# Optimization experiments

Measured on AMD Instinct MI355X. Metric: run time of the kernel, lower is better.

## Reference

```python
import jax, jax.numpy as jnp
import numpy as np
from functools import partial

FEAT = 12544  # 64 * 14 * 14, CfC input_size
UNITS = 64
BB = 128      # ncps CfC default backbone_units (backbone_layers=1)
N_ACTIONS = 8


def lecun_tanh(x):
    return 1.7159 * jnp.tanh(0.666 * x)


def setup_inputs() -> dict:
    key = jax.random.key(0)
    ks = jax.random.split(key, 20)
    s = 0.05
    inp = {
        "x": jax.random.normal(ks[0], (16, 64, 3, 62, 62), dtype=jnp.float32),
        "conv1_w": jax.random.normal(ks[1], (32, 3, 4, 4), dtype=jnp.float32) * s,
        "conv1_b": jnp.zeros((32,), dtype=jnp.float32),
        "conv2_w": jax.random.normal(ks[2], (64, 32, 4, 4), dtype=jnp.float32) * s,
        "conv2_b": jnp.zeros((64,), dtype=jnp.float32),
        "W_bb": jax.random.normal(ks[3], (FEAT + UNITS, BB), dtype=jnp.float32) * 0.01,
        "b_bb": jnp.zeros((BB,), dtype=jnp.float32),
        "W_ff1": jax.random.normal(ks[4], (BB, UNITS), dtype=jnp.float32) * s,
        "b_ff1": jnp.zeros((UNITS,), dtype=jnp.float32),
        "W_ff2": jax.random.normal(ks[5], (BB, UNITS), dtype=jnp.float32) * s,
        "b_ff2": jnp.zeros((UNITS,), dtype=jnp.float32),
        "W_ta": jax.random.normal(ks[6], (BB, UNITS), dtype=jnp.float32) * s,
        "b_ta": jnp.zeros((UNITS,), dtype=jnp.float32),
        "W_tb": jax.random.normal(ks[7], (BB, UNITS), dtype=jnp.float32) * s,
        "b_tb": jnp.zeros((UNITS,), dtype=jnp.float32),
        "W_out": jax.random.normal(ks[8], (UNITS, N_ACTIONS), dtype=jnp.float32) * s,
        "b_out": jnp.zeros((N_ACTIONS,), dtype=jnp.float32),
    }
    return inp


def _conv(x, w, b):
    y = jax.lax.conv_general_dilated(
        x, w, window_strides=(2, 2), padding="VALID",
        dimension_numbers=("NCHW", "OIHW", "NCHW"))
    return jax.nn.relu(y + b[None, :, None, None])


def reference(x, conv1_w, conv1_b, conv2_w, conv2_b, W_bb, b_bb,
              W_ff1, b_ff1, W_ff2, b_ff2, W_ta, b_ta, W_tb, b_tb,
              W_out, b_out):
    B, T, C, H, W = x.shape
    c_in = x.reshape(B * T, C, H, W)
    h = _conv(c_in, conv1_w, conv1_b)          # [BT,32,30,30]
    h = _conv(h, conv2_w, conv2_b)             # [BT,64,14,14]
    feat = h.reshape(B, T, FEAT)               # torch Flatten order == NCHW reshape

    # CfC (ncps, mode='default', backbone_layers=1, ts=1.0), return_sequences=False
    W_in, W_h = W_bb[:FEAT], W_bb[FEAT:]
    # precompute input contribution to backbone for all timesteps
    u = jnp.einsum("btf,fk->btk", feat, W_in) + b_bb   # [B,T,BB]

    def step(hid, u_t):
        z = lecun_tanh(u_t + hid @ W_h)                # backbone activation
        ff1 = jnp.tanh(z @ W_ff1 + b_ff1)
        ff2 = jnp.tanh(z @ W_ff2 + b_ff2)
        t_interp = jax.nn.sigmoid((z @ W_ta + b_ta) + (z @ W_tb + b_tb))  # ts=1.0
        hid_new = ff1 * (1.0 - t_interp) + t_interp * ff2
        return hid_new, None

    h0 = jnp.zeros((B, UNITS), dtype=x.dtype)
    h_last, _ = jax.lax.scan(step, h0, jnp.swapaxes(u, 0, 1))  # scan over time
    return h_last @ W_out + b_out
```

## Files before the change

### kernel.cpp

```cpp
#include <hip/hip_runtime.h>
#include <hip/hip_bf16.h>
#include <math.h>

#define FEATN 12544
#define NIMG 1024
#define PLANEP 482

typedef __attribute__((ext_vector_type(8))) short short8;
typedef __attribute__((ext_vector_type(4))) float f32x4;

#define OFF_W1F   0
#define OFF_W2F   6144
#define OFF_WBBF  71680
#define OFF_FEATB 62265344
#define OFF_U     87955456
#define OFF_PART  88479744
#define OFF_WHF   103163904
#define OFF_WGF   103180288
#define WS_BYTES  103245824

__device__ __forceinline__ unsigned short f2bf(float v) {
    union { float f; unsigned int u; } c; c.f = v;
    unsigned int r = c.u + 0x7FFFu + ((c.u >> 16) & 1u);
    return (unsigned short)(r >> 16);
}
__device__ __forceinline__ unsigned short f2bf_rhu(float v) {
    union { float f; unsigned int u; } c; c.f = v;
    return (unsigned short)((c.u + 0x8000u) >> 16);
}
__device__ __forceinline__ unsigned int pack2bf_rhu(float lo, float hi) {
    union { float f; unsigned int u; } a, b; a.f = lo; b.f = hi;
    return ((a.u + 0x8000u) >> 16) | ((b.u + 0x8000u) & 0xFFFF0000u);
}

__device__ __forceinline__ float lecun_tanh_fast(float x) {
    float e = __builtin_amdgcn_exp2f(1.9216698f * x);
    return 1.7159f - 3.4318f * __builtin_amdgcn_rcpf(e + 1.f);
}
__device__ __forceinline__ float tanh_fast(float x) {
    float e = __builtin_amdgcn_exp2f(2.8853901f * x);
    return 1.f - 2.f * __builtin_amdgcn_rcpf(e + 1.f);
}
__device__ __forceinline__ float sigmoid_fast(float x) {
    float e = __builtin_amdgcn_exp2f(-1.4426950f * x);
    return __builtin_amdgcn_rcpf(1.f + e);
}

__global__ __launch_bounds__(256) void prep_all(const float* __restrict__ w1, const float* __restrict__ w2,
                         const float* __restrict__ Wbb,
                         const float* __restrict__ Wff1, const float* __restrict__ Wff2,
                         const float* __restrict__ Wta,  const float* __restrict__ Wtb,
                         unsigned short* __restrict__ w1f, unsigned short* __restrict__ w2f,
                         unsigned short* __restrict__ wbbf,
                         unsigned short* __restrict__ whf, unsigned short* __restrict__ wgf) {
    int bid = blockIdx.x, tid = threadIdx.x;
    if (bid < 6272) {
        int i = bid * 256 + tid;
        int j = i & 7, lane = (i >> 3) & 63, nt = (i >> 9) & 7, kstep = i >> 12;
        int f = kstep * 32 + (lane >> 4) * 8 + j;
        int col = nt * 16 + (lane & 15);
        wbbf[i] = f2bf(Wbb[(size_t)f * 128 + col]);
    } else if (bid < 6400) {
        int i = (bid - 6272) * 256 + tid;
        int j = i & 7, lane = (i >> 3) & 63, kstep = (i >> 9) & 15, nt = i >> 13;
        int oc = nt * 16 + (lane & 15);
        int ic = 2 * kstep + (j >> 2);
        int ky = lane >> 4, kx = j & 3;
        w2f[i] = f2bf(w2[oc * 512 + ic * 16 + ky * 4 + kx]);
    } else if (bid < 6528) {
        int i = (bid - 6400) * 256 + tid;
        int j = i & 7, lane = (i >> 3) & 63, nt = (i >> 9) & 15, kstep = (i >> 13) & 3;
        int gq = (lane >> 4) & 3;
        int k = kstep * 32 + (j & 1) * 16 + gq * 4 + (j >> 1);
        int m = nt >> 2;
        int c = (nt & 3) * 16 + (lane & 15);
        float v;
        if (m == 0)      v = Wff1[k * 64 + c];
        else if (m == 1) v = Wff2[k * 64 + c];
        else if (m == 2) v = Wta[k * 64 + c] + Wtb[k * 64 + c];
        else             v = 0.f;
        wgf[i] = f2bf(v);
    } else if (bid < 6560) {
        int i = (bid - 6528) * 256 + tid;
        int j = i & 7, lane = (i >> 3) & 63, nt = (i >> 9) & 7, kstep = (i >> 12) & 1;
        int k = kstep * 32 + ((lane >> 4) & 3) * 8 + j;
        int col = nt * 16 + (lane & 15);
        whf[i] = f2bf(Wbb[(size_t)(FEATN + k) * 128 + col]);
    } else {
        int i = (bid - 6560) * 256 + tid;
        if (i >= 2048) return;
        int j = i & 7, lane = (i >> 3) & 63, nt = (i >> 9) & 1, kstep = (i >> 10) & 1;
        int oc = nt * 16 + (lane & 15);
        int ky = (lane >> 4) & 3, kx = j & 3;
        float v;
        if (kstep == 0) { int ic = j >> 2; v = w1[oc * 48 + ic * 16 + ky * 4 + kx]; }
        else            { v = (j >> 2) == 0 ? w1[oc * 48 + 32 + ky * 4 + kx] : 0.f; }
        w1f[i] = f2bf(v);
    }
}

__global__ __launch_bounds__(512) void fused_conv(const float* __restrict__ x,
                                                  const float* __restrict__ b1,
                                                  const unsigned short* __restrict__ w1f,
                                                  const float* __restrict__ b2,
                                                  const unsigned short* __restrict__ w2f,
                                                  unsigned short* __restrict__ featb) {
    __shared__ unsigned short h1s[32 * 2 * PLANEP];
    int img = blockIdx.x;
    int tid = threadIdx.x;
    int lane = tid & 63, wid = tid >> 6;
    int rowl = lane & 15, g = lane >> 4;
    const float* xg = x + (size_t)img * 11532;

    {
        short8 bfr[2][2];
        #pragma unroll
        for (int ks = 0; ks < 2; ++ks)
            #pragma unroll
            for (int nt = 0; nt < 2; ++nt)
                bfr[ks][nt] = *(const short8*)(w1f + (((ks * 2 + nt) * 64 + lane) << 3));
        float bias0 = b1[rowl], bias1 = b1[16 + rowl];

        #pragma unroll
        for (int i = 0; i < 8; ++i) {
            int mtile = wid + 8 * i;
            if (mtile >= 57) break;
            int m = mtile * 16 + rowl; if (m > 899) m = 899;
            int oy = m / 30, ox = m - oy * 30;
            int y = 2 * oy + g, x0 = 2 * ox;
            const float* xb = xg + y * 62 + x0;
            union { unsigned int u[4]; short8 s; } af0, af1;
            #pragma unroll
            for (int c = 0; c < 2; ++c) {
                float2 p0 = *(const float2*)(xb + c * 3844);
                float2 p1 = *(const float2*)(xb + c * 3844 + 2);
                af0.u[c * 2]     = pack2bf_rhu(p0.x, p0.y);
                af0.u[c * 2 + 1] = pack2bf_rhu(p1.x, p1.y);
            }
            {
                float2 q0 = *(const float2*)(xb + 7688);
                float2 q1 = *(const float2*)(xb + 7690);
                af1.u[0] = pack2bf_rhu(q0.x, q0.y);
                af1.u[1] = pack2bf_rhu(q1.x, q1.y);
                af1.u[2] = 0; af1.u[3] = 0;
            }
            f32x4 acc0 = (f32x4){0.f, 0.f, 0.f, 0.f};
            f32x4 acc1 = (f32x4){0.f, 0.f, 0.f, 0.f};
            acc0 = __builtin_amdgcn_mfma_f32_16x16x32_bf16(af0.s, bfr[0][0], acc0, 0, 0, 0);
            acc0 = __builtin_amdgcn_mfma_f32_16x16x32_bf16(af1.s, bfr[1][0], acc0, 0, 0, 0);
            acc1 = __builtin_amdgcn_mfma_f32_16x16x32_bf16(af0.s, bfr[0][1], acc1, 0, 0, 0);
            acc1 = __builtin_amdgcn_mfma_f32_16x16x32_bf16(af1.s, bfr[1][1], acc1, 0, 0, 0);
            int sp0 = mtile * 16 + g * 4;
            int oy0 = sp0 / 30, ox0 = sp0 - oy0 * 30;
            #pragma unroll
            for (int nt = 0; nt < 2; ++nt) {
                f32x4 a = nt ? acc1 : acc0;
                int oc = nt * 16 + rowl;
                float bias = nt ? bias1 : bias0;
                int pbase = oc * (2 * PLANEP);
                #pragma unroll
                for (int r = 0; r < 4; ++r) {
                    if (sp0 + r > 899) break;
                    int oxr = ox0 + r, oyr = oy0;
                    if (oxr >= 30) { oxr -= 30; ++oyr; }
                    h1s[pbase + oyr * 32 + oxr] = f2bf_rhu(fmaxf(a[r] + bias, 0.f));
                }
            }
        }
    }
    __syncthreads();

    f32x4 acc[2][4];
    #pragma unroll
    for (int i = 0; i < 2; ++i)
        #pragma unroll
        for (int nt = 0; nt < 4; ++nt) acc[i][nt] = (f32x4){0.f, 0.f, 0.f, 0.f};

    int dofs[2];
    #pragma unroll
    for (int i = 0; i < 2; ++i) {
        int mtile = wid + 8 * i;
        int m = mtile * 16 + rowl; if (m > 195) m = 195;
        int oy = m / 14, ox = m - oy * 14;
        int y = 2 * oy + g, x0 = 2 * ox;
        dofs[i] = y * 16 + (x0 >> 1);
    }
    const unsigned int* lds32 = (const unsigned int*)h1s;

    #pragma unroll 4
    for (int kstep = 0; kstep < 16; ++kstep) {
        short8 bfr[4];
        #pragma unroll
        for (int nt = 0; nt < 4; ++nt)
            bfr[nt] = *(const short8*)(w2f + (((nt * 16 + kstep) * 64 + lane) << 3));
        int icb = kstep * 2 * PLANEP;
        #pragma unroll
        for (int i = 0; i < 2; ++i) {
            int mtile = wid + 8 * i;
            if (mtile < 13) {
                int dof = icb + dofs[i];
                union { unsigned int u[4]; short8 s; } af;
                af.u[0] = lds32[dof];
                af.u[1] = lds32[dof + 1];
                af.u[2] = lds32[dof + PLANEP];
                af.u[3] = lds32[dof + PLANEP + 1];
                #pragma unroll
                for (int nt = 0; nt < 4; ++nt)
                    acc[i][nt] = __builtin_amdgcn_mfma_f32_16x16x32_bf16(af.s, bfr[nt], acc[i][nt], 0, 0, 0);
            }
        }
    }
    #pragma unroll
    for (int i = 0; i < 2; ++i) {
        int mtile = wid + 8 * i;
        if (mtile >= 13) continue;
        int sp0 = mtile * 16 + g * 4;
        #pragma unroll
        for (int nt = 0; nt < 4; ++nt) {
            int oc = nt * 16 + rowl;
            float bias = b2[oc];
            unsigned short pk[4];
            #pragma unroll
            for (int r = 0; r < 4; ++r)
                pk[r] = f2bf_rhu(fmaxf(acc[i][nt][r] + bias, 0.f));
            unsigned short* dstp = featb + (size_t)img * 12544 + oc * 196 + sp0;
            if (sp0 + 3 < 196) {
                *(uint2*)dstp = *(uint2*)pk;
            } else {
                #pragma unroll
                for (int r = 0; r < 4; ++r) if (sp0 + r < 196) dstp[r] = pk[r];
            }
        }
    }
}

__global__ __launch_bounds__(256) void gemm_u_mfma(const unsigned short* __restrict__ featb,
                                                   const unsigned short* __restrict__ Wbbf,
                                                   float* __restrict__ part) {
    int tid = threadIdx.x, lane = tid & 63, wid = tid >> 6;
    int rowl = lane & 15, g = lane >> 4;
    int m0 = blockIdx.x * 64 + wid * 16;
    int ks0 = blockIdx.y * 14;
    f32x4 acc[8];
    #pragma unroll
    for (int nt = 0; nt < 8; ++nt) acc[nt] = (f32x4){0.f, 0.f, 0.f, 0.f};
    const unsigned short* arow = featb + (size_t)(m0 + rowl) * FEATN + g * 8;
    #pragma unroll 2
    for (int kk = 0; kk < 14; ++kk) {
        int kstep = ks0 + kk;
        short8 afr = *(const short8*)(arow + kstep * 32);
        #pragma unroll
        for (int nt = 0; nt < 8; ++nt) {
            short8 bfr = *(const short8*)(Wbbf + ((((size_t)kstep * 8 + nt) * 64 + lane) << 3));
            acc[nt] = __builtin_amdgcn_mfma_f32_16x16x32_bf16(afr, bfr, acc[nt], 0, 0, 0);
        }
    }
    float* pg = part + (size_t)blockIdx.y * 131072;
    #pragma unroll
    for (int nt = 0; nt < 8; ++nt)
        #pragma unroll
        for (int r = 0; r < 4; ++r)
            pg[(m0 + g * 4 + r) * 128 + nt * 16 + rowl] = acc[nt][r];
}

__global__ void reduce_u(const float4* __restrict__ part4, const float* __restrict__ bbb,
                         float* __restrict__ u) {
    int o = blockIdx.x * 256 + threadIdx.x;
    int c4 = o & 31, b = (o >> 5) & 15, t = o >> 9;
    int m = b * 64 + t;
    float4 s = *(const float4*)(bbb + c4 * 4);
    #pragma unroll
    for (int ks = 0; ks < 28; ++ks) {
        float4 p = part4[(size_t)ks * 32768 + m * 32 + c4];
        s.x += p.x; s.y += p.y; s.z += p.z; s.w += p.w;
    }
    int cb = c4 * 4;
    u[((size_t)t * 128 + cb + 0) * 16 + b] = s.x;
    u[((size_t)t * 128 + cb + 1) * 16 + b] = s.y;
    u[((size_t)t * 128 + cb + 2) * 16 + b] = s.z;
    u[((size_t)t * 128 + cb + 3) * 16 + b] = s.w;
}

__global__ __launch_bounds__(256, 1) void rnn_mfma(const float* __restrict__ u,
                                                   const unsigned short* __restrict__ whf,
                                                   const unsigned short* __restrict__ wgf,
                                                   const float* __restrict__ bff1,
                                                   const float* __restrict__ bff2,
                                                   const float* __restrict__ bta,
                                                   const float* __restrict__ btb,
                                                   const float* __restrict__ Wout,
                                                   const float* __restrict__ bout,
                                                   float* __restrict__ out) {
    __shared__ unsigned short hidA[16 * 64];
    __shared__ unsigned short zA[16 * 128];
    int tid = threadIdx.x, lane = tid & 63, w = tid >> 6;
    int rowl = lane & 15, g = lane >> 4;

    for (int idx = tid; idx < 1024; idx += 256) hidA[idx] = 0;

    short8 wh_r[2][2];
    #pragma unroll
    for (int ks = 0; ks < 2; ++ks)
        #pragma unroll
        for (int ntl = 0; ntl < 2; ++ntl)
            wh_r[ks][ntl] = *(const short8*)(whf + (((ks * 8 + 2 * w + ntl) * 64 + lane) << 3));
    short8 wg_r[3][4];
    #pragma unroll
    for (int m = 0; m < 3; ++m)
        #pragma unroll
        for (int ks = 0; ks < 4; ++ks)
            wg_r[m][ks] = *(const short8*)(wgf + (((ks * 16 + 4 * m + w) * 64 + lane) << 3));

    int cc = w * 16 + rowl;
    float bias1 = bff1[cc], bias2 = bff2[cc], biast = bta[cc] + btb[cc];

    const float* ub0 = u + ((size_t)(2 * w) * 16 + rowl) * 16 + g * 4;
    const float* ub1 = u + ((size_t)(2 * w + 1) * 16 + rowl) * 16 + g * 4;
    f32x4 upf[2];
    {
        float4 v0 = *(const float4*)ub0;
        float4 v1 = *(const float4*)ub1;
        upf[0] = (f32x4){v0.x, v0.y, v0.z, v0.w};
        upf[1] = (f32x4){v1.x, v1.y, v1.z, v1.w};
    }
    __syncthreads();

    float hidv[4];
    #pragma unroll 1
    for (int t = 0; t < 64; ++t) {
        short8 ah[2];
        #pragma unroll
        for (int ks = 0; ks < 2; ++ks) {
            int byte = (rowl * 128 + ks * 64 + g * 16) ^ ((rowl & 7) << 4);
            ah[ks] = *(const short8*)((const char*)hidA + byte);
        }
        f32x4 zacc[2];
        #pragma unroll
        for (int ntl = 0; ntl < 2; ++ntl) {
            zacc[ntl] = upf[ntl];
            #pragma unroll
            for (int ks = 0; ks < 2; ++ks)
                zacc[ntl] = __builtin_amdgcn_mfma_f32_16x16x32_bf16(ah[ks], wh_r[ks][ntl], zacc[ntl], 0, 0, 0);
        }
        if (t < 63) {
            float4 v0 = *(const float4*)(ub0 + (size_t)(t + 1) * 2048);
            float4 v1 = *(const float4*)(ub1 + (size_t)(t + 1) * 2048);
            upf[0] = (f32x4){v0.x, v0.y, v0.z, v0.w};
            upf[1] = (f32x4){v1.x, v1.y, v1.z, v1.w};
        }
        #pragma unroll
        for (int r = 0; r < 4; ++r) {
            float z0 = lecun_tanh_fast(zacc[0][r]);
            float z1 = lecun_tanh_fast(zacc[1][r]);
            int row = g * 4 + r;
            int byte = (row * 256 + w * 64 + rowl * 4) ^ ((row & 7) << 4);
            *(unsigned int*)((char*)zA + byte) = pack2bf_rhu(z0, z1);
        }
        __syncthreads();
        short8 zfr[4];
        #pragma unroll
        for (int ks = 0; ks < 4; ++ks) {
            int byte = (rowl * 256 + ks * 64 + g * 16) ^ ((rowl & 7) << 4);
            zfr[ks] = *(const short8*)((const char*)zA + byte);
        }
        f32x4 facc[3];
        facc[0] = (f32x4){bias1, bias1, bias1, bias1};
        facc[1] = (f32x4){bias2, bias2, bias2, bias2};
        facc[2] = (f32x4){biast, biast, biast, biast};
        #pragma unroll
        for (int m = 0; m < 3; ++m)
            #pragma unroll
            for (int ks = 0; ks < 4; ++ks)
                facc[m] = __builtin_amdgcn_mfma_f32_16x16x32_bf16(zfr[ks], wg_r[m][ks], facc[m], 0, 0, 0);
        #pragma unroll
        for (int r = 0; r < 4; ++r) {
            float ff1 = tanh_fast(facc[0][r]);
            float ff2 = tanh_fast(facc[1][r]);
            float tt  = sigmoid_fast(facc[2][r]);
            float hv  = ff1 + tt * (ff2 - ff1);
            hidv[r] = hv;
            int row = g * 4 + r;
            int byte = (row * 128 + cc * 2) ^ ((row & 7) << 4);
            *(unsigned short*)((char*)hidA + byte) = f2bf_rhu(hv);
        }
        __syncthreads();
    }

    float* hf = (float*)zA;
    #pragma unroll
    for (int r = 0; r < 4; ++r) hf[(g * 4 + r) * 64 + cc] = hidv[r];
    __syncthreads();
    if (tid < 128) {
        int b = tid >> 3, a = tid & 7;
        float s = bout[a];
        #pragma unroll
        for (int j = 0; j < 64; ++j) s += hf[b * 64 + j] * Wout[j * 8 + a];
        out[tid] = s;
    }
}

extern "C" void kernel_launch(void* const* d_in, const int* in_sizes, int n_in,
                              void* d_out, int out_size, void* d_ws, size_t ws_size,
                              hipStream_t stream) {
    const float* x    = (const float*)d_in[0];
    const float* w1   = (const float*)d_in[1];
    const float* b1   = (const float*)d_in[2];
    const float* w2   = (const float*)d_in[3];
    const float* b2   = (const float*)d_in[4];
    const float* Wbb  = (const float*)d_in[5];
    const float* bbb  = (const float*)d_in[6];
    const float* Wff1 = (const float*)d_in[7];
    const float* bff1 = (const float*)d_in[8];
    const float* Wff2 = (const float*)d_in[9];
    const float* bff2 = (const float*)d_in[10];
    const float* Wta  = (const float*)d_in[11];
    const float* bta  = (const float*)d_in[12];
    const float* Wtb  = (const float*)d_in[13];
    const float* btb  = (const float*)d_in[14];
    const float* Wout = (const float*)d_in[15];
    const float* bout = (const float*)d_in[16];

    if (ws_size < (size_t)WS_BYTES) return;

    char* wsb = (char*)d_ws;
    unsigned short* w1f   = (unsigned short*)(wsb + OFF_W1F);
    unsigned short* w2f   = (unsigned short*)(wsb + OFF_W2F);
    unsigned short* wbbf  = (unsigned short*)(wsb + OFF_WBBF);
    unsigned short* featb = (unsigned short*)(wsb + OFF_FEATB);
    float*          u     = (float*)(wsb + OFF_U);
    float*          part  = (float*)(wsb + OFF_PART);
    unsigned short* whf   = (unsigned short*)(wsb + OFF_WHF);
    unsigned short* wgf   = (unsigned short*)(wsb + OFF_WGF);

    prep_all<<<6568, 256, 0, stream>>>(w1, w2, Wbb, Wff1, Wff2, Wta, Wtb,
                                       w1f, w2f, wbbf, whf, wgf);
    fused_conv<<<1024, 512, 0, stream>>>(x, b1, w1f, b2, w2f, featb);
    gemm_u_mfma<<<dim3(16, 28), 256, 0, stream>>>(featb, wbbf, part);
    reduce_u<<<128, 256, 0, stream>>>((const float4*)part, bbb, u);
    rnn_mfma<<<1, 256, 0, stream>>>(u, whf, wgf, bff1, bff2, bta, btb, Wout, bout, (float*)d_out);
}
```

Before: 115.3 us.

## Split fused conv per image into two half-height blocks

Each image's fused conv1+conv2 is now split across two blocks, each handling half the conv2 output rows (7 of 14) and the 16 conv1 rows those need. The LDS footprint per block is roughly halved (PLANE2 instead of PLANEP), and the grid doubles to 2048 blocks, which is meant to raise occupancy and parallelism. In exchange, each half recomputes the overlapping conv1 rows, and only 7 of 8 waves do work in the conv2 phase.

```diff
diff --git a/kernel.cpp b/kernel.cpp
--- a/kernel.cpp
+++ b/kernel.cpp
@@ -4,7 +4,7 @@
 
 #define FEATN 12544
 #define NIMG 1024
-#define PLANEP 482
+#define PLANE2 258
 
 typedef __attribute__((ext_vector_type(8))) short short8;
 typedef __attribute__((ext_vector_type(4))) float f32x4;
@@ -105,8 +105,9 @@
                                                   const float* __restrict__ b2,
                                                   const unsigned short* __restrict__ w2f,
                                                   unsigned short* __restrict__ featb) {
-    __shared__ unsigned short h1s[32 * 2 * PLANEP];
-    int img = blockIdx.x;
+    __shared__ unsigned short h1s[32 * 2 * PLANE2];
+    int img = blockIdx.x >> 1;
+    int h   = blockIdx.x & 1;
     int tid = threadIdx.x;
     int lane = tid & 63, wid = tid >> 6;
     int rowl = lane & 15, g = lane >> 4;
@@ -122,13 +123,13 @@
         float bias0 = b1[rowl], bias1 = b1[16 + rowl];
 
         #pragma unroll
-        for (int i = 0; i < 8; ++i) {
+        for (int i = 0; i < 4; ++i) {
             int mtile = wid + 8 * i;
-            if (mtile >= 57) break;
-            int m = mtile * 16 + rowl; if (m > 899) m = 899;
-            int oy = m / 30, ox = m - oy * 30;
-            int y = 2 * oy + g, x0 = 2 * ox;
-            const float* xb = xg + y * 62 + x0;
+            if (mtile >= 30) break;
+            int m = mtile * 16 + rowl; if (m > 479) m = 479;
+            int ly = m / 30, ox = m - ly * 30;
+            int yx = 28 * h + 2 * ly + g;
+            const float* xb = xg + yx * 62 + 2 * ox;
             union { unsigned int u[4]; short8 s; } af0, af1;
             #pragma unroll
             for (int c = 0; c < 2; ++c) {
@@ -151,70 +152,54 @@
             acc1 = __builtin_amdgcn_mfma_f32_16x16x32_bf16(af0.s, bfr[0][1], acc1, 0, 0, 0);
             acc1 = __builtin_amdgcn_mfma_f32_16x16x32_bf16(af1.s, bfr[1][1], acc1, 0, 0, 0);
             int sp0 = mtile * 16 + g * 4;
-            int oy0 = sp0 / 30, ox0 = sp0 - oy0 * 30;
+            int ly0 = sp0 / 30, ox0 = sp0 - ly0 * 30;
             #pragma unroll
             for (int nt = 0; nt < 2; ++nt) {
                 f32x4 a = nt ? acc1 : acc0;
                 int oc = nt * 16 + rowl;
                 float bias = nt ? bias1 : bias0;
-                int pbase = oc * (2 * PLANEP);
+                int pbase = oc * (2 * PLANE2);
                 #pragma unroll
                 for (int r = 0; r < 4; ++r) {
-                    if (sp0 + r > 899) break;
-                    int oxr = ox0 + r, oyr = oy0;
-                    if (oxr >= 30) { oxr -= 30; ++oyr; }
-                    h1s[pbase + oyr * 32 + oxr] = f2bf_rhu(fmaxf(a[r] + bias, 0.f));
+                    if (sp0 + r > 479) break;
+                    int oxr = ox0 + r, lyr = ly0;
+                    if (oxr >= 30) { oxr -= 30; ++lyr; }
+                    h1s[pbase + lyr * 32 + oxr] = f2bf_rhu(fmaxf(a[r] + bias, 0.f));
                 }
             }
         }
     }
     __syncthreads();
 
-    f32x4 acc[2][4];
-    #pragma unroll
-    for (int i = 0; i < 2; ++i)
-        #pragma unroll
-        for (int nt = 0; nt < 4; ++nt) acc[i][nt] = (f32x4){0.f, 0.f, 0.f, 0.f};
-
-    int dofs[2];
-    #pragma unroll
-    for (int i = 0; i < 2; ++i) {
-        int mtile = wid + 8 * i;
-        int m = mtile * 16 + rowl; if (m > 195) m = 195;
-        int oy = m / 14, ox = m - oy * 14;
-        int y = 2 * oy + g, x0 = 2 * ox;
-        dofs[i] = y * 16 + (x0 >> 1);
-    }
-    const unsigned int* lds32 = (const unsigned int*)h1s;
-
-    #pragma unroll 4
-    for (int kstep = 0; kstep < 16; ++kstep) {
-        short8 bfr[4];
-        #pragma unroll
-        for (int nt = 0; nt < 4; ++nt)
-            bfr[nt] = *(const short8*)(w2f + (((nt * 16 + kstep) * 64 + lane) << 3));
-        int icb = kstep * 2 * PLANEP;
-        #pragma unroll
-        for (int i = 0; i < 2; ++i) {
-            int mtile = wid + 8 * i;
-            if (mtile < 13) {
-                int dof = icb + dofs[i];
-                union { unsigned int u[4]; short8 s; } af;
-                af.u[0] = lds32[dof];
-                af.u[1] = lds32[dof + 1];
-                af.u[2] = lds32[dof + PLANEP];
-                af.u[3] = lds32[dof + PLANEP + 1];
-                #pragma unroll
-                for (int nt = 0; nt < 4; ++nt)
-                    acc[i][nt] = __builtin_amdgcn_mfma_f32_16x16x32_bf16(af.s, bfr[nt], acc[i][nt], 0, 0, 0);
-            }
-        }
-    }
-    #pragma unroll
-    for (int i = 0; i < 2; ++i) {
-        int mtile = wid + 8 * i;
-        if (mtile >= 13) continue;
-        int sp0 = mtile * 16 + g * 4;
+    if (wid < 7) {
+        int mtile = wid;
+        f32x4 acc[4];
+        #pragma unroll
+        for (int nt = 0; nt < 4; ++nt) acc[nt] = (f32x4){0.f, 0.f, 0.f, 0.f};
+
+        int m = mtile * 16 + rowl; if (m > 97) m = 97;
+        int oyl = m / 14, ox = m - oyl * 14;
+        int dof0 = (2 * oyl + g) * 16 + ox;
+        const unsigned int* lds32 = (const unsigned int*)h1s;
+
+        #pragma unroll 4
+        for (int kstep = 0; kstep < 16; ++kstep) {
+            short8 bfr[4];
+            #pragma unroll
+            for (int nt = 0; nt < 4; ++nt)
+                bfr[nt] = *(const short8*)(w2f + (((nt * 16 + kstep) * 64 + lane) << 3));
+            int dof = kstep * 2 * PLANE2 + dof0;
+            union { unsigned int u[4]; short8 s; } af;
+            af.u[0] = lds32[dof];
+            af.u[1] = lds32[dof + 1];
+            af.u[2] = lds32[dof + PLANE2];
+            af.u[3] = lds32[dof + PLANE2 + 1];
+            #pragma unroll
+            for (int nt = 0; nt < 4; ++nt)
+                acc[nt] = __builtin_amdgcn_mfma_f32_16x16x32_bf16(af.s, bfr[nt], acc[nt], 0, 0, 0);
+        }
+        int spl0 = mtile * 16 + g * 4;
+        int spg0 = h * 98 + spl0;
         #pragma unroll
         for (int nt = 0; nt < 4; ++nt) {
             int oc = nt * 16 + rowl;
@@ -222,13 +207,14 @@
             unsigned short pk[4];
             #pragma unroll
             for (int r = 0; r < 4; ++r)
-                pk[r] = f2bf_rhu(fmaxf(acc[i][nt][r] + bias, 0.f));
-            unsigned short* dstp = featb + (size_t)img * 12544 + oc * 196 + sp0;
-            if (sp0 + 3 < 196) {
-                *(uint2*)dstp = *(uint2*)pk;
+                pk[r] = f2bf_rhu(fmaxf(acc[nt][r] + bias, 0.f));
+            unsigned short* dstp = featb + (size_t)img * 12544 + oc * 196 + spg0;
+            if (spl0 + 3 <= 97) {
+                ((unsigned int*)dstp)[0] = (unsigned int)pk[0] | ((unsigned int)pk[1] << 16);
+                ((unsigned int*)dstp)[1] = (unsigned int)pk[2] | ((unsigned int)pk[3] << 16);
             } else {
                 #pragma unroll
-                for (int r = 0; r < 4; ++r) if (sp0 + r < 196) dstp[r] = pk[r];
+                for (int r = 0; r < 4; ++r) if (spl0 + r <= 97) dstp[r] = pk[r];
             }
         }
     }
@@ -434,7 +420,7 @@
 
     prep_all<<<6568, 256, 0, stream>>>(w1, w2, Wbb, Wff1, Wff2, Wta, Wtb,
                                        w1f, w2f, wbbf, whf, wgf);
-    fused_conv<<<1024, 512, 0, stream>>>(x, b1, w1f, b2, w2f, featb);
+    fused_conv<<<2048, 512, 0, stream>>>(x, b1, w1f, b2, w2f, featb);
     gemm_u_mfma<<<dim3(16, 28), 256, 0, stream>>>(featb, wbbf, part);
     reduce_u<<<128, 256, 0, stream>>>((const float4*)part, bbb, u);
     rnn_mfma<<<1, 256, 0, stream>>>(u, whf, wgf, bff1, bff2, bta, btb, Wout, bout, (float*)d_out);
```

New measurement: 127.6 us. +10.7%, slower.

## Fuse conv, backbone GEMM and RNN into one persistent kernel with flag sync

Applied to the files above, without the earlier changes.

Merges the conv, input-projection GEMM, partial reduce and recurrent scan into a single launch. Conv blocks are reordered by timestep and bump a per-timestep counter. GEMM blocks wait on that counter and then publish a ready index in order. The RNN block consumes timesteps as they become ready. This is meant to overlap the serial recurrence with feature and GEMM production and to drop three launches plus the partial-sum buffer. The risks are deadlock if the spinning blocks are not co-resident with their producers, and much less GEMM parallelism: 64 blocks, each doing the full K of one timestep.

```diff
diff --git a/kernel.cpp b/kernel.cpp
--- a/kernel.cpp
+++ b/kernel.cpp
@@ -14,10 +14,10 @@
 #define OFF_WBBF  71680
 #define OFF_FEATB 62265344
 #define OFF_U     87955456
-#define OFF_PART  88479744
 #define OFF_WHF   103163904
 #define OFF_WGF   103180288
-#define WS_BYTES  103245824
+#define OFF_FLAGS 103245824
+#define WS_BYTES  103246592
 
 __device__ __forceinline__ unsigned short f2bf(float v) {
     union { float f; unsigned int u; } c; c.f = v;
@@ -52,7 +52,8 @@
                          const float* __restrict__ Wta,  const float* __restrict__ Wtb,
                          unsigned short* __restrict__ w1f, unsigned short* __restrict__ w2f,
                          unsigned short* __restrict__ wbbf,
-                         unsigned short* __restrict__ whf, unsigned short* __restrict__ wgf) {
+                         unsigned short* __restrict__ whf, unsigned short* __restrict__ wgf,
+                         unsigned int* __restrict__ flags) {
     int bid = blockIdx.x, tid = threadIdx.x;
     if (bid < 6272) {
         int i = bid * 256 + tid;
@@ -86,7 +87,7 @@
         int k = kstep * 32 + ((lane >> 4) & 3) * 8 + j;
         int col = nt * 16 + (lane & 15);
         whf[i] = f2bf(Wbb[(size_t)(FEATN + k) * 128 + col]);
-    } else {
+    } else if (bid < 6568) {
         int i = (bid - 6560) * 256 + tid;
         if (i >= 2048) return;
         int j = i & 7, lane = (i >> 3) & 63, nt = (i >> 9) & 1, kstep = (i >> 10) & 1;
@@ -96,306 +97,326 @@
         if (kstep == 0) { int ic = j >> 2; v = w1[oc * 48 + ic * 16 + ky * 4 + kx]; }
         else            { v = (j >> 2) == 0 ? w1[oc * 48 + 32 + ky * 4 + kx] : 0.f; }
         w1f[i] = f2bf(v);
+    } else {
+        if (tid < 192) flags[tid] = 0;
     }
 }
 
-__global__ __launch_bounds__(512) void fused_conv(const float* __restrict__ x,
-                                                  const float* __restrict__ b1,
-                                                  const unsigned short* __restrict__ w1f,
-                                                  const float* __restrict__ b2,
-                                                  const unsigned short* __restrict__ w2f,
-                                                  unsigned short* __restrict__ featb) {
-    __shared__ unsigned short h1s[32 * 2 * PLANEP];
-    int img = blockIdx.x;
+__global__ __launch_bounds__(512) void fused_net(const float* __restrict__ x,
+                        const float* __restrict__ b1, const unsigned short* __restrict__ w1f,
+                        const float* __restrict__ b2, const unsigned short* __restrict__ w2f,
+                        unsigned short* __restrict__ featb,
+                        const unsigned short* __restrict__ Wbbf, const float* __restrict__ bbb,
+                        float* __restrict__ u,
+                        const unsigned short* __restrict__ whf, const unsigned short* __restrict__ wgf,
+                        const float* __restrict__ bff1, const float* __restrict__ bff2,
+                        const float* __restrict__ bta,  const float* __restrict__ btb,
+                        const float* __restrict__ Wout, const float* __restrict__ bout,
+                        float* __restrict__ out,
+                        unsigned int* __restrict__ cnt, unsigned int* __restrict__ ready) {
+    __shared__ char smem[61696];
+    int bid = blockIdx.x;
     int tid = threadIdx.x;
     int lane = tid & 63, wid = tid >> 6;
     int rowl = lane & 15, g = lane >> 4;
-    const float* xg = x + (size_t)img * 11532;
-
-    {
-        short8 bfr[2][2];
-        #pragma unroll
-        for (int ks = 0; ks < 2; ++ks)
-            #pragma unroll
-            for (int nt = 0; nt < 2; ++nt)
-                bfr[ks][nt] = *(const short8*)(w1f + (((ks * 2 + nt) * 64 + lane) << 3));
-        float bias0 = b1[rowl], bias1 = b1[16 + rowl];
-
-        #pragma unroll
-        for (int i = 0; i < 8; ++i) {
-            int mtile = wid + 8 * i;
-            if (mtile >= 57) break;
-            int m = mtile * 16 + rowl; if (m > 899) m = 899;
-            int oy = m / 30, ox = m - oy * 30;
-            int y = 2 * oy + g, x0 = 2 * ox;
-            const float* xb = xg + y * 62 + x0;
-            union { unsigned int u[4]; short8 s; } af0, af1;
-            #pragma unroll
-            for (int c = 0; c < 2; ++c) {
-                float2 p0 = *(const float2*)(xb + c * 3844);
-                float2 p1 = *(const float2*)(xb + c * 3844 + 2);
-                af0.u[c * 2]     = pack2bf_rhu(p0.x, p0.y);
-                af0.u[c * 2 + 1] = pack2bf_rhu(p1.x, p1.y);
-            }
-            {
-                float2 q0 = *(const float2*)(xb + 7688);
-                float2 q1 = *(const float2*)(xb + 7690);
-                af1.u[0] = pack2bf_rhu(q0.x, q0.y);
-                af1.u[1] = pack2bf_rhu(q1.x, q1.y);
-                af1.u[2] = 0; af1.u[3] = 0;
-            }
-            f32x4 acc0 = (f32x4){0.f, 0.f, 0.f, 0.f};
-            f32x4 acc1 = (f32x4){0.f, 0.f, 0.f, 0.f};
-            acc0 = __builtin_amdgcn_mfma_f32_16x16x32_bf16(af0.s, bfr[0][0], acc0, 0, 0, 0);
-            acc0 = __builtin_amdgcn_mfma_f32_16x16x32_bf16(af1.s, bfr[1][0], acc0, 0, 0, 0);
-            acc1 = __builtin_amdgcn_mfma_f32_16x16x32_bf16(af0.s, bfr[0][1], acc1, 0, 0, 0);
-            acc1 = __builtin_amdgcn_mfma_f32_16x16x32_bf16(af1.s, bfr[1][1], acc1, 0, 0, 0);
-            int sp0 = mtile * 16 + g * 4;
-            int oy0 = sp0 / 30, ox0 = sp0 - oy0 * 30;
-            #pragma unroll
-            for (int nt = 0; nt < 2; ++nt) {
-                f32x4 a = nt ? acc1 : acc0;
-                int oc = nt * 16 + rowl;
-                float bias = nt ? bias1 : bias0;
-                int pbase = oc * (2 * PLANEP);
-                #pragma unroll
-                for (int r = 0; r < 4; ++r) {
-                    if (sp0 + r > 899) break;
-                    int oxr = ox0 + r, oyr = oy0;
-                    if (oxr >= 30) { oxr -= 30; ++oyr; }
-                    h1s[pbase + oyr * 32 + oxr] = f2bf_rhu(fmaxf(a[r] + bias, 0.f));
+
+    if (bid < 1024) {
+        int tt = bid >> 4;
+        int img = (bid & 15) * 64 + tt;
+        unsigned short* h1s = (unsigned short*)smem;
+        const float* xg = x + (size_t)img * 11532;
+        {
+            short8 bfr[2][2];
+            #pragma unroll
+            for (int ks = 0; ks < 2; ++ks)
+                #pragma unroll
+                for (int nt = 0; nt < 2; ++nt)
+                    bfr[ks][nt] = *(const short8*)(w1f + (((ks * 2 + nt) * 64 + lane) << 3));
+            float bias0 = b1[rowl], bias1 = b1[16 + rowl];
+
+            #pragma unroll
+            for (int i = 0; i < 8; ++i) {
+                int mtile = wid + 8 * i;
+                if (mtile >= 57) break;
+                int m = mtile * 16 + rowl; if (m > 899) m = 899;
+                int oy = m / 30, ox = m - oy * 30;
+                int y = 2 * oy + g, x0 = 2 * ox;
+                const float* xb = xg + y * 62 + x0;
+                union { unsigned int uu[4]; short8 s; } af0, af1;
+                #pragma unroll
+                for (int c = 0; c < 2; ++c) {
+                    float2 p0 = *(const float2*)(xb + c * 3844);
+                    float2 p1 = *(const float2*)(xb + c * 3844 + 2);
+                    af0.uu[c * 2]     = pack2bf_rhu(p0.x, p0.y);
+                    af0.uu[c * 2 + 1] = pack2bf_rhu(p1.x, p1.y);
                 }
-            }
-        }
-    }
-    __syncthreads();
-
-    f32x4 acc[2][4];
-    #pragma unroll
-    for (int i = 0; i < 2; ++i)
-        #pragma unroll
-        for (int nt = 0; nt < 4; ++nt) acc[i][nt] = (f32x4){0.f, 0.f, 0.f, 0.f};
-
-    int dofs[2];
-    #pragma unroll
-    for (int i = 0; i < 2; ++i) {
-        int mtile = wid + 8 * i;
-        int m = mtile * 16 + rowl; if (m > 195) m = 195;
-        int oy = m / 14, ox = m - oy * 14;
-        int y = 2 * oy + g, x0 = 2 * ox;
-        dofs[i] = y * 16 + (x0 >> 1);
-    }
-    const unsigned int* lds32 = (const unsigned int*)h1s;
-
-    #pragma unroll 4
-    for (int kstep = 0; kstep < 16; ++kstep) {
-        short8 bfr[4];
-        #pragma unroll
-        for (int nt = 0; nt < 4; ++nt)
-            bfr[nt] = *(const short8*)(w2f + (((nt * 16 + kstep) * 64 + lane) << 3));
-        int icb = kstep * 2 * PLANEP;
+                {
+                    float2 q0 = *(const float2*)(xb + 7688);
+                    float2 q1 = *(const float2*)(xb + 7690);
+                    af1.uu[0] = pack2bf_rhu(q0.x, q0.y);
+                    af1.uu[1] = pack2bf_rhu(q1.x, q1.y);
+                    af1.uu[2] = 0; af1.uu[3] = 0;
+                }
+                f32x4 acc0 = (f32x4){0.f, 0.f, 0.f, 0.f};
+                f32x4 acc1 = (f32x4){0.f, 0.f, 0.f, 0.f};
+                acc0 = __builtin_amdgcn_mfma_f32_16x16x32_bf16(af0.s, bfr[0][0], acc0, 0, 0, 0);
+                acc0 = __builtin_amdgcn_mfma_f32_16x16x32_bf16(af1.s, bfr[1][0], acc0, 0, 0, 0);
+                acc1 = __builtin_amdgcn_mfma_f32_16x16x32_bf16(af0.s, bfr[0][1], acc1, 0, 0, 0);
+                acc1 = __builtin_amdgcn_mfma_f32_16x16x32_bf16(af1.s, bfr[1][1], acc1, 0, 0, 0);
+                int sp0 = mtile * 16 + g * 4;
+                int oy0 = sp0 / 30, ox0 = sp0 - oy0 * 30;
+                #pragma unroll
+                for (int nt = 0; nt < 2; ++nt) {
+                    f32x4 a = nt ? acc1 : acc0;
+                    int oc = nt * 16 + rowl;
+                    float bias = nt ? bias1 : bias0;
+                    int pbase = oc * (2 * PLANEP);
+                    #pragma unroll
+                    for (int r = 0; r < 4; ++r) {
+                        if (sp0 + r > 899) break;
+                        int oxr = ox0 + r, oyr = oy0;
+                        if (oxr >= 30) { oxr -= 30; ++oyr; }
+                        h1s[pbase + oyr * 32 + oxr] = f2bf_rhu(fmaxf(a[r] + bias, 0.f));
+                    }
+                }
+            }
+        }
+        __syncthreads();
+
+        f32x4 acc[2][4];
+        #pragma unroll
+        for (int i = 0; i < 2; ++i)
+            #pragma unroll
+            for (int nt = 0; nt < 4; ++nt) acc[i][nt] = (f32x4){0.f, 0.f, 0.f, 0.f};
+        int dofs[2];
         #pragma unroll
         for (int i = 0; i < 2; ++i) {
             int mtile = wid + 8 * i;
-            if (mtile < 13) {
-                int dof = icb + dofs[i];
-                union { unsigned int u[4]; short8 s; } af;
-                af.u[0] = lds32[dof];
-                af.u[1] = lds32[dof + 1];
-                af.u[2] = lds32[dof + PLANEP];
-                af.u[3] = lds32[dof + PLANEP + 1];
-                #pragma unroll
-                for (int nt = 0; nt < 4; ++nt)
-                    acc[i][nt] = __builtin_amdgcn_mfma_f32_16x16x32_bf16(af.s, bfr[nt], acc[i][nt], 0, 0, 0);
-            }
-        }
-    }
-    #pragma unroll
-    for (int i = 0; i < 2; ++i) {
-        int mtile = wid + 8 * i;
-        if (mtile >= 13) continue;
-        int sp0 = mtile * 16 + g * 4;
-        #pragma unroll
-        for (int nt = 0; nt < 4; ++nt) {
-            int oc = nt * 16 + rowl;
-            float bias = b2[oc];
-            unsigned short pk[4];
+            int m = mtile * 16 + rowl; if (m > 195) m = 195;
+            int oy = m / 14, ox = m - oy * 14;
+            int y = 2 * oy + g, x0 = 2 * ox;
+            dofs[i] = y * 16 + (x0 >> 1);
+        }
+        const unsigned int* lds32 = (const unsigned int*)h1s;
+        #pragma unroll 4
+        for (int kstep = 0; kstep < 16; ++kstep) {
+            short8 bfr[4];
+            #pragma unroll
+            for (int nt = 0; nt < 4; ++nt)
+                bfr[nt] = *(const short8*)(w2f + (((nt * 16 + kstep) * 64 + lane) << 3));
+            int icb = kstep * 2 * PLANEP;
+            #pragma unroll
+            for (int i = 0; i < 2; ++i) {
+                int mtile = wid + 8 * i;
+                if (mtile < 13) {
+                    int dof = icb + dofs[i];
+                    union { unsigned int uu[4]; short8 s; } af;
+                    af.uu[0] = lds32[dof];
+                    af.uu[1] = lds32[dof + 1];
+                    af.uu[2] = lds32[dof + PLANEP];
+                    af.uu[3] = lds32[dof + PLANEP + 1];
+                    #pragma unroll
+                    for (int nt = 0; nt < 4; ++nt)
+                        acc[i][nt] = __builtin_amdgcn_mfma_f32_16x16x32_bf16(af.s, bfr[nt], acc[i][nt], 0, 0, 0);
+                }
+            }
+        }
+        #pragma unroll
+        for (int i = 0; i < 2; ++i) {
+            int mtile = wid + 8 * i;
+            if (mtile >= 13) continue;
+            int sp0 = mtile * 16 + g * 4;
+            #pragma unroll
+            for (int nt = 0; nt < 4; ++nt) {
+                int oc = nt * 16 + rowl;
+                float bias = b2[oc];
+                unsigned short pk[4];
+                #pragma unroll
+                for (int r = 0; r < 4; ++r)
+                    pk[r] = f2bf_rhu(fmaxf(acc[i][nt][r] + bias, 0.f));
+                unsigned short* dstp = featb + (size_t)img * 12544 + oc * 196 + sp0;
+                if (sp0 + 3 < 196) {
+                    *(uint2*)dstp = *(uint2*)pk;
+                } else {
+                    #pragma unroll
+                    for (int r = 0; r < 4; ++r) if (sp0 + r < 196) dstp[r] = pk[r];
+                }
+            }
+        }
+        __syncthreads();
+        if (tid == 0) {
+            __threadfence();
+            __hip_atomic_fetch_add(&cnt[tt], 1u, __ATOMIC_RELEASE, __HIP_MEMORY_SCOPE_AGENT);
+        }
+    } else if (bid < 1088) {
+        const int t = bid - 1024;
+        while (__hip_atomic_load(&cnt[t], __ATOMIC_RELAXED, __HIP_MEMORY_SCOPE_AGENT) < 16u)
+            __builtin_amdgcn_s_sleep(32);
+        __threadfence();
+
+        int kw = wid & 3, nh = wid >> 2;
+        f32x4 acc[4];
+        #pragma unroll
+        for (int ntl = 0; ntl < 4; ++ntl) acc[ntl] = (f32x4){0.f, 0.f, 0.f, 0.f};
+        const unsigned short* arow = featb + (size_t)(rowl * 64 + t) * FEATN + g * 8;
+        int ks0 = kw * 98;
+        #pragma unroll 2
+        for (int kk = 0; kk < 98; ++kk) {
+            int kstep = ks0 + kk;
+            short8 afr = *(const short8*)(arow + kstep * 32);
+            #pragma unroll
+            for (int ntl = 0; ntl < 4; ++ntl) {
+                short8 bfr = *(const short8*)(Wbbf + ((((size_t)kstep * 8 + nh * 4 + ntl) * 64 + lane) << 3));
+                acc[ntl] = __builtin_amdgcn_mfma_f32_16x16x32_bf16(afr, bfr, acc[ntl], 0, 0, 0);
+            }
+        }
+        float* red = (float*)smem;
+        #pragma unroll
+        for (int ntl = 0; ntl < 4; ++ntl)
             #pragma unroll
             for (int r = 0; r < 4; ++r)
-                pk[r] = f2bf_rhu(fmaxf(acc[i][nt][r] + bias, 0.f));
-            unsigned short* dstp = featb + (size_t)img * 12544 + oc * 196 + sp0;
-            if (sp0 + 3 < 196) {
-                *(uint2*)dstp = *(uint2*)pk;
-            } else {
-                #pragma unroll
-                for (int r = 0; r < 4; ++r) if (sp0 + r < 196) dstp[r] = pk[r];
-            }
-        }
-    }
-}
-
-__global__ __launch_bounds__(256) void gemm_u_mfma(const unsigned short* __restrict__ featb,
-                                                   const unsigned short* __restrict__ Wbbf,
-                                                   float* __restrict__ part) {
-    int tid = threadIdx.x, lane = tid & 63, wid = tid >> 6;
-    int rowl = lane & 15, g = lane >> 4;
-    int m0 = blockIdx.x * 64 + wid * 16;
-    int ks0 = blockIdx.y * 14;
-    f32x4 acc[8];
-    #pragma unroll
-    for (int nt = 0; nt < 8; ++nt) acc[nt] = (f32x4){0.f, 0.f, 0.f, 0.f};
-    const unsigned short* arow = featb + (size_t)(m0 + rowl) * FEATN + g * 8;
-    #pragma unroll 2
-    for (int kk = 0; kk < 14; ++kk) {
-        int kstep = ks0 + kk;
-        short8 afr = *(const short8*)(arow + kstep * 32);
-        #pragma unroll
-        for (int nt = 0; nt < 8; ++nt) {
-            short8 bfr = *(const short8*)(Wbbf + ((((size_t)kstep * 8 + nt) * 64 + lane) << 3));
-            acc[nt] = __builtin_amdgcn_mfma_f32_16x16x32_bf16(afr, bfr, acc[nt], 0, 0, 0);
-        }
-    }
-    float* pg = part + (size_t)blockIdx.y * 131072;
-    #pragma unroll
-    for (int nt = 0; nt < 8; ++nt)
-        #pragma unroll
-        for (int r = 0; r < 4; ++r)
-            pg[(m0 + g * 4 + r) * 128 + nt * 16 + rowl] = acc[nt][r];
-}
-
-__global__ void reduce_u(const float4* __restrict__ part4, const float* __restrict__ bbb,
-                         float* __restrict__ u) {
-    int o = blockIdx.x * 256 + threadIdx.x;
-    int c4 = o & 31, b = (o >> 5) & 15, t = o >> 9;
-    int m = b * 64 + t;
-    float4 s = *(const float4*)(bbb + c4 * 4);
-    #pragma unroll
-    for (int ks = 0; ks < 28; ++ks) {
-        float4 p = part4[(size_t)ks * 32768 + m * 32 + c4];
-        s.x += p.x; s.y += p.y; s.z += p.z; s.w += p.w;
-    }
-    int cb = c4 * 4;
-    u[((size_t)t * 128 + cb + 0) * 16 + b] = s.x;
-    u[((size_t)t * 128 + cb + 1) * 16 + b] = s.y;
-    u[((size_t)t * 128 + cb + 2) * 16 + b] = s.z;
-    u[((size_t)t * 128 + cb + 3) * 16 + b] = s.w;
-}
-
-__global__ __launch_bounds__(256, 1) void rnn_mfma(const float* __restrict__ u,
-                                                   const unsigned short* __restrict__ whf,
-                                                   const unsigned short* __restrict__ wgf,
-                                                   const float* __restrict__ bff1,
-                                                   const float* __restrict__ bff2,
-                                                   const float* __restrict__ bta,
-                                                   const float* __restrict__ btb,
-                                                   const float* __restrict__ Wout,
-                                                   const float* __restrict__ bout,
-                                                   float* __restrict__ out) {
-    __shared__ unsigned short hidA[16 * 64];
-    __shared__ unsigned short zA[16 * 128];
-    int tid = threadIdx.x, lane = tid & 63, w = tid >> 6;
-    int rowl = lane & 15, g = lane >> 4;
-
-    for (int idx = tid; idx < 1024; idx += 256) hidA[idx] = 0;
-
-    short8 wh_r[2][2];
-    #pragma unroll
-    for (int ks = 0; ks < 2; ++ks)
-        #pragma unroll
-        for (int ntl = 0; ntl < 2; ++ntl)
-            wh_r[ks][ntl] = *(const short8*)(whf + (((ks * 8 + 2 * w + ntl) * 64 + lane) << 3));
-    short8 wg_r[3][4];
-    #pragma unroll
-    for (int m = 0; m < 3; ++m)
-        #pragma unroll
-        for (int ks = 0; ks < 4; ++ks)
-            wg_r[m][ks] = *(const short8*)(wgf + (((ks * 16 + 4 * m + w) * 64 + lane) << 3));
-
-    int cc = w * 16 + rowl;
-    float bias1 = bff1[cc], bias2 = bff2[cc], biast = bta[cc] + btb[cc];
-
-    const float* ub0 = u + ((size_t)(2 * w) * 16 + rowl) * 16 + g * 4;
-    const float* ub1 = u + ((size_t)(2 * w + 1) * 16 + rowl) * 16 + g * 4;
-    f32x4 upf[2];
-    {
-        float4 v0 = *(const float4*)ub0;
-        float4 v1 = *(const float4*)ub1;
-        upf[0] = (f32x4){v0.x, v0.y, v0.z, v0.w};
-        upf[1] = (f32x4){v1.x, v1.y, v1.z, v1.w};
-    }
-    __syncthreads();
-
-    float hidv[4];
-    #pragma unroll 1
-    for (int t = 0; t < 64; ++t) {
-        short8 ah[2];
-        #pragma unroll
-        for (int ks = 0; ks < 2; ++ks) {
-            int byte = (rowl * 128 + ks * 64 + g * 16) ^ ((rowl & 7) << 4);
-            ah[ks] = *(const short8*)((const char*)hidA + byte);
-        }
-        f32x4 zacc[2];
-        #pragma unroll
-        for (int ntl = 0; ntl < 2; ++ntl) {
-            zacc[ntl] = upf[ntl];
-            #pragma unroll
-            for (int ks = 0; ks < 2; ++ks)
-                zacc[ntl] = __builtin_amdgcn_mfma_f32_16x16x32_bf16(ah[ks], wh_r[ks][ntl], zacc[ntl], 0, 0, 0);
-        }
-        if (t < 63) {
-            float4 v0 = *(const float4*)(ub0 + (size_t)(t + 1) * 2048);
-            float4 v1 = *(const float4*)(ub1 + (size_t)(t + 1) * 2048);
+                red[wid * 1024 + (g * 4 + r) * 64 + ntl * 16 + rowl] = acc[ntl][r];
+        __syncthreads();
+        #pragma unroll
+        for (int q = 0; q < 4; ++q) {
+            int o = tid + q * 512;
+            int b = o & 15, c = o >> 4;
+            int lcol = c & 63, nho = c >> 6;
+            float s = bbb[c];
+            #pragma unroll
+            for (int k2 = 0; k2 < 4; ++k2)
+                s += red[(nho * 4 + k2) * 1024 + b * 64 + lcol];
+            u[(size_t)t * 2048 + o] = s;
+        }
+        __syncthreads();
+        if (tid == 0) {
+            __threadfence();
+            while (__hip_atomic_load(ready, __ATOMIC_RELAXED, __HIP_MEMORY_SCOPE_AGENT) != (unsigned)t)
+                __builtin_amdgcn_s_sleep(16);
+            __hip_atomic_store(ready, (unsigned)(t + 1), __ATOMIC_RELEASE, __HIP_MEMORY_SCOPE_AGENT);
+        }
+    } else {
+        if (wid >= 4) {
+            for (int i = 0; i < 130; ++i) __syncthreads();
+            return;
+        }
+        unsigned short* hidA = (unsigned short*)smem;
+        unsigned short* zA   = (unsigned short*)(smem + 2048);
+        int w = wid;
+
+        for (int idx = tid; idx < 1024; idx += 256) hidA[idx] = 0;
+
+        short8 wh_r[2][2];
+        #pragma unroll
+        for (int ks = 0; ks < 2; ++ks)
+            #pragma unroll
+            for (int ntl = 0; ntl < 2; ++ntl)
+                wh_r[ks][ntl] = *(const short8*)(whf + (((ks * 8 + 2 * w + ntl) * 64 + lane) << 3));
+        short8 wg_r[3][4];
+        #pragma unroll
+        for (int m = 0; m < 3; ++m)
+            #pragma unroll
+            for (int ks = 0; ks < 4; ++ks)
+                wg_r[m][ks] = *(const short8*)(wgf + (((ks * 16 + 4 * m + w) * 64 + lane) << 3));
+
+        int cc = w * 16 + rowl;
+        float bias1 = bff1[cc], bias2 = bff2[cc], biast = bta[cc] + btb[cc];
+
+        const float* ub0 = u + ((size_t)(2 * w) * 16 + rowl) * 16 + g * 4;
+        const float* ub1 = u + ((size_t)(2 * w + 1) * 16 + rowl) * 16 + g * 4;
+
+#define WAIT_READY(n) do { \
+        while (__hip_atomic_load(ready, __ATOMIC_RELAXED, __HIP_MEMORY_SCOPE_AGENT) < (unsigned)(n)) \
+            __builtin_amdgcn_s_sleep(32); \
+        __threadfence(); } while (0)
+
+        WAIT_READY(1);
+        f32x4 upf[2];
+        {
+            float4 v0 = *(const float4*)ub0;
+            float4 v1 = *(const float4*)ub1;
             upf[0] = (f32x4){v0.x, v0.y, v0.z, v0.w};
             upf[1] = (f32x4){v1.x, v1.y, v1.z, v1.w};
         }
-        #pragma unroll
-        for (int r = 0; r < 4; ++r) {
-            float z0 = lecun_tanh_fast(zacc[0][r]);
-            float z1 = lecun_tanh_fast(zacc[1][r]);
-            int row = g * 4 + r;
-            int byte = (row * 256 + w * 64 + rowl * 4) ^ ((row & 7) << 4);
-            *(unsigned int*)((char*)zA + byte) = pack2bf_rhu(z0, z1);
-        }
-        __syncthreads();
-        short8 zfr[4];
-        #pragma unroll
-        for (int ks = 0; ks < 4; ++ks) {
-            int byte = (rowl * 256 + ks * 64 + g * 16) ^ ((rowl & 7) << 4);
-            zfr[ks] = *(const short8*)((const char*)zA + byte);
-        }
-        f32x4 facc[3];
-        facc[0] = (f32x4){bias1, bias1, bias1, bias1};
-        facc[1] = (f32x4){bias2, bias2, bias2, bias2};
-        facc[2] = (f32x4){biast, biast, biast, biast};
-        #pragma unroll
-        for (int m = 0; m < 3; ++m)
-            #pragma unroll
-            for (int ks = 0; ks < 4; ++ks)
-                facc[m] = __builtin_amdgcn_mfma_f32_16x16x32_bf16(zfr[ks], wg_r[m][ks], facc[m], 0, 0, 0);
-        #pragma unroll
-        for (int r = 0; r < 4; ++r) {
-            float ff1 = tanh_fast(facc[0][r]);
-            float ff2 = tanh_fast(facc[1][r]);
-            float tt  = sigmoid_fast(facc[2][r]);
-            float hv  = ff1 + tt * (ff2 - ff1);
-            hidv[r] = hv;
-            int row = g * 4 + r;
-            int byte = (row * 128 + cc * 2) ^ ((row & 7) << 4);
-            *(unsigned short*)((char*)hidA + byte) = f2bf_rhu(hv);
-        }
-        __syncthreads();
-    }
-
-    float* hf = (float*)zA;
-    #pragma unroll
-    for (int r = 0; r < 4; ++r) hf[(g * 4 + r) * 64 + cc] = hidv[r];
-    __syncthreads();
-    if (tid < 128) {
-        int b = tid >> 3, a = tid & 7;
-        float s = bout[a];
-        #pragma unroll
-        for (int j = 0; j < 64; ++j) s += hf[b * 64 + j] * Wout[j * 8 + a];
-        out[tid] = s;
+        __syncthreads();
+
+        float hidv[4];
+        #pragma unroll 1
+        for (int t = 0; t < 64; ++t) {
+            if ((t & 7) == 0) {
+                int need = t + 9; if (need > 64) need = 64;
+                WAIT_READY(need);
+            }
+            short8 ah[2];
+            #pragma unroll
+            for (int ks = 0; ks < 2; ++ks) {
+                int byte = (rowl * 128 + ks * 64 + g * 16) ^ ((rowl & 7) << 4);
+                ah[ks] = *(const short8*)((const char*)hidA + byte);
+            }
+            f32x4 zacc[2];
+            #pragma unroll
+            for (int ntl = 0; ntl < 2; ++ntl) {
+                zacc[ntl] = upf[ntl];
+                #pragma unroll
+                for (int ks = 0; ks < 2; ++ks)
+                    zacc[ntl] = __builtin_amdgcn_mfma_f32_16x16x32_bf16(ah[ks], wh_r[ks][ntl], zacc[ntl], 0, 0, 0);
+            }
+            if (t < 63) {
+                float4 v0 = *(const float4*)(ub0 + (size_t)(t + 1) * 2048);
+                float4 v1 = *(const float4*)(ub1 + (size_t)(t + 1) * 2048);
+                upf[0] = (f32x4){v0.x, v0.y, v0.z, v0.w};
+                upf[1] = (f32x4){v1.x, v1.y, v1.z, v1.w};
+            }
+            #pragma unroll
+            for (int r = 0; r < 4; ++r) {
+                float z0 = lecun_tanh_fast(zacc[0][r]);
+                float z1 = lecun_tanh_fast(zacc[1][r]);
+                int row = g * 4 + r;
+                int byte = (row * 256 + w * 64 + rowl * 4) ^ ((row & 7) << 4);
+                *(unsigned int*)((char*)zA + byte) = pack2bf_rhu(z0, z1);
+            }
+            __syncthreads();
+            short8 zfr[4];
+            #pragma unroll
+            for (int ks = 0; ks < 4; ++ks) {
+                int byte = (rowl * 256 + ks * 64 + g * 16) ^ ((rowl & 7) << 4);
+                zfr[ks] = *(const short8*)((const char*)zA + byte);
+            }
+            f32x4 facc[3];
+            facc[0] = (f32x4){bias1, bias1, bias1, bias1};
+            facc[1] = (f32x4){bias2, bias2, bias2, bias2};
+            facc[2] = (f32x4){biast, biast, biast, biast};
+            #pragma unroll
+            for (int m = 0; m < 3; ++m)
+                #pragma unroll
+                for (int ks = 0; ks < 4; ++ks)
+                    facc[m] = __builtin_amdgcn_mfma_f32_16x16x32_bf16(zfr[ks], wg_r[m][ks], facc[m], 0, 0, 0);
+            #pragma unroll
+            for (int r = 0; r < 4; ++r) {
+                float ff1 = tanh_fast(facc[0][r]);
+                float ff2 = tanh_fast(facc[1][r]);
+                float ttv = sigmoid_fast(facc[2][r]);
+                float hv  = ff1 + ttv * (ff2 - ff1);
+                hidv[r] = hv;
+                int row = g * 4 + r;
+                int byte = (row * 128 + cc * 2) ^ ((row & 7) << 4);
+                *(unsigned short*)((char*)hidA + byte) = f2bf_rhu(hv);
+            }
+            __syncthreads();
+        }
+
+        float* hf = (float*)zA;
+        #pragma unroll
+        for (int r = 0; r < 4; ++r) hf[(g * 4 + r) * 64 + cc] = hidv[r];
+        __syncthreads();
+        if (tid < 128) {
+            int b = tid >> 3, a = tid & 7;
+            float s = bout[a];
+            #pragma unroll
+            for (int j = 0; j < 64; ++j) s += hf[b * 64 + j] * Wout[j * 8 + a];
+            out[tid] = s;
+        }
+#undef WAIT_READY
     }
 }
 
@@ -428,14 +449,16 @@
     unsigned short* wbbf  = (unsigned short*)(wsb + OFF_WBBF);
     unsigned short* featb = (unsigned short*)(wsb + OFF_FEATB);
     float*          u     = (float*)(wsb + OFF_U);
-    float*          part  = (float*)(wsb + OFF_PART);
     unsigned short* whf   = (unsigned short*)(wsb + OFF_WHF);
     unsigned short* wgf   = (unsigned short*)(wsb + OFF_WGF);
-
-    prep_all<<<6568, 256, 0, stream>>>(w1, w2, Wbb, Wff1, Wff2, Wta, Wtb,
-                                       w1f, w2f, wbbf, whf, wgf);
-    fused_conv<<<1024, 512, 0, stream>>>(x, b1, w1f, b2, w2f, featb);
-    gemm_u_mfma<<<dim3(16, 28), 256, 0, stream>>>(featb, wbbf, part);
-    reduce_u<<<128, 256, 0, stream>>>((const float4*)part, bbb, u);
-    rnn_mfma<<<1, 256, 0, stream>>>(u, whf, wgf, bff1, bff2, bta, btb, Wout, bout, (float*)d_out);
-}
+    unsigned int*   flags = (unsigned int*)(wsb + OFF_FLAGS);
+    unsigned int*   cnt   = flags;
+    unsigned int*   ready = flags + 64;
+
+    prep_all<<<6569, 256, 0, stream>>>(w1, w2, Wbb, Wff1, Wff2, Wta, Wtb,
+                                       w1f, w2f, wbbf, whf, wgf, flags);
+    fused_net<<<1089, 512, 0, stream>>>(x, b1, w1f, b2, w2f, featb,
+                                        wbbf, bbb, u, whf, wgf,
+                                        bff1, bff2, bta, btb, Wout, bout,
+                                        (float*)d_out, cnt, ready);
+}
```

Measured after the change: 260.3 us. 126% more time.
